# Performance work log

Hardware: AMD Instinct MI355X
Metric: run time of the kernel (lower is better)

Reference implementation:

```python
import math
import jax, jax.numpy as jnp
import numpy as np

LAMBDA_INIT = 0.8
GN_EPS = 1e-5

B, H, S, D = 2, 16, 2048, 128  # batch, heads, seq, head_dim


def setup_inputs() -> dict:
    key = jax.random.key(0)
    ks = jax.random.split(key, 8)
    return {
        "q": jax.random.normal(ks[0], (B, H, S, 2 * D), dtype=jnp.float32),
        "k": jax.random.normal(ks[1], (B, H, S, 2 * D), dtype=jnp.float32),
        "v": jax.random.normal(ks[2], (B, H, S, D), dtype=jnp.float32),
        "lam_q1": jax.random.normal(ks[3], (D,), dtype=jnp.float32),
        "lam_q2": jax.random.normal(ks[4], (D,), dtype=jnp.float32),
        "lam_k1": jax.random.normal(ks[5], (D,), dtype=jnp.float32),
        "lam_k2": jax.random.normal(ks[6], (D,), dtype=jnp.float32),
        "gn_weight": jnp.ones((H * D,), dtype=jnp.float32),
        "gn_bias": jnp.zeros((H * D,), dtype=jnp.float32),
    }


def reference(q, k, v, lam_q1, lam_q2, lam_k1, lam_k2, gn_weight, gn_bias):
    d = q.shape[-1] // 2
    scale = 1.0 / math.sqrt(d)
    Q1, Q2 = q[..., :d], q[..., d:]
    K1, K2 = k[..., :d], k[..., d:]
    # dual score matrices [B,H,S,S]
    w1 = jax.nn.softmax(jnp.einsum('bhsd,bhtd->bhst', Q1, K1) * scale, axis=-1)
    w2 = jax.nn.softmax(jnp.einsum('bhsd,bhtd->bhst', Q2, K2) * scale, axis=-1)
    lam = jnp.exp(jnp.dot(lam_q1, lam_k1)) - jnp.exp(jnp.dot(lam_q2, lam_k2)) + LAMBDA_INIT
    weights = w1 - lam * w2
    out = jnp.einsum('bhst,bhtd->bhsd', weights, v)  # [B,H,S,D]
    # GroupNorm(num_groups=H, num_channels=H*D) applied on [B, H*D, S]:
    # channel c = h*D + dd, normalization per (batch, head) over (D, S).
    mean = out.mean(axis=(2, 3), keepdims=True)
    var = out.var(axis=(2, 3), keepdims=True)
    normed = (out - mean) * jax.lax.rsqrt(var + GN_EPS)
    gamma = gn_weight.reshape(1, out.shape[1], 1, d)
    beta = gn_bias.reshape(1, out.shape[1], 1, d)
    return (normed * gamma + beta) * (1.0 - LAMBDA_INIT)
```

## Files before the change

kernel.cpp:

```cpp
#include <hip/hip_runtime.h>
#include <cstddef>

constexpr int B = 2, H = 16, S = 2048, D = 128;
constexpr int BH = B * H;
constexpr int TWOD = 2 * D;
constexpr int QTILE = 128;
constexpr int BC = 32;
constexpr int NKT = S / BC;
constexpr float SC2 = 0.08838834764831845f * 1.4426950408889634f;
constexpr float LAM_INIT = 0.8f;
constexpr float GN_EPS = 1e-5f;

typedef __attribute__((ext_vector_type(8))) short short8;
typedef __attribute__((ext_vector_type(4))) float f32x4;

__device__ __forceinline__ unsigned short f2b(float f) {
  unsigned int u = __float_as_uint(f);
  u += 0x7fffu + ((u >> 16) & 1u);
  return (unsigned short)(u >> 16);
}

__device__ __forceinline__ void async_copy16(const void* g, void* l) {
  typedef __attribute__((address_space(1))) const void gvoid;
  typedef __attribute__((address_space(3))) void lvoid;
  __builtin_amdgcn_global_load_lds((gvoid*)g, (lvoid*)l, 16, 0, 0);
}

__global__ void lam_kernel(const float* __restrict__ lq1, const float* __restrict__ lq2,
                           const float* __restrict__ lk1, const float* __restrict__ lk2,
                           float* __restrict__ wsf) {
  __shared__ float r1[128], r2[128];
  int t = threadIdx.x;
  r1[t] = lq1[t] * lk1[t];
  r2[t] = lq2[t] * lk2[t];
  __syncthreads();
  if (t == 0) {
    float s1 = 0.f, s2 = 0.f;
    for (int i = 0; i < 128; ++i) { s1 += r1[i]; s2 += r2[i]; }
    wsf[0] = expf(s1) - expf(s2) + LAM_INIT;
  }
}

__global__ void convk_kernel(const float* __restrict__ src, unsigned short* __restrict__ dst) {
  size_t i = ((size_t)blockIdx.x * 256 + threadIdx.x) * 8;
  float4 a = *(const float4*)(src + i);
  float4 b = *(const float4*)(src + i + 4);
  unsigned short u[8];
  u[0] = f2b(a.x); u[1] = f2b(a.y); u[2] = f2b(a.z); u[3] = f2b(a.w);
  u[4] = f2b(b.x); u[5] = f2b(b.y); u[6] = f2b(b.z); u[7] = f2b(b.w);
  *(uint4*)(dst + i) = *(uint4*)u;
}

__global__ void vt_kernel(const float* __restrict__ v, unsigned short* __restrict__ vtg) {
  __shared__ float tile[64][129];
  const int bh = blockIdx.y, s0 = blockIdx.x * 64, t = threadIdx.x;
#pragma unroll
  for (int i = 0; i < 8; ++i) {
    int idx = t + i * 256;
    int row = idx >> 5, c4 = idx & 31;
    float4 f = *(const float4*)(v + ((size_t)bh * S + s0 + row) * D + c4 * 4);
    tile[row][c4 * 4 + 0] = f.x; tile[row][c4 * 4 + 1] = f.y;
    tile[row][c4 * 4 + 2] = f.z; tile[row][c4 * 4 + 3] = f.w;
  }
  __syncthreads();
#pragma unroll
  for (int i = 0; i < 4; ++i) {
    int c = t + i * 256;
    int d = c >> 3, k8 = c & 7;
    unsigned short u[8];
#pragma unroll
    for (int j = 0; j < 8; ++j) u[j] = f2b(tile[k8 * 8 + j][d]);
    *(uint4*)(vtg + ((size_t)bh * D + d) * S + s0 + k8 * 8) = *(uint4*)u;
  }
}

__global__ __launch_bounds__(256, 2)
void attn_kernel(const float* __restrict__ q, const unsigned short* __restrict__ kbf,
                 const unsigned short* __restrict__ vtg,
                 float* __restrict__ wsf, float* __restrict__ out) {
  __shared__ __attribute__((aligned(16))) unsigned short Ks[2][32][256];
  __shared__ __attribute__((aligned(16))) unsigned short Vt[2][128][40];
  __shared__ __attribute__((aligned(16))) unsigned short Pa[4][2][32][40];
  __shared__ float sred[4][2];

  const int bh = blockIdx.x, qb = blockIdx.y;
  const int q0 = qb * QTILE;
  const int tid = threadIdx.x;
  const int wave = tid >> 6, lane = tid & 63;
  const int quad = lane >> 4, l16 = lane & 15;
  const float lam = wsf[0];

  short8 qf[2][2][4];
#pragma unroll
  for (int mt = 0; mt < 2; ++mt) {
    int qrow = q0 + wave * 32 + mt * 16 + l16;
    const float* qr = q + ((size_t)bh * S + qrow) * TWOD;
#pragma unroll
    for (int st = 0; st < 2; ++st)
#pragma unroll
      for (int ks = 0; ks < 4; ++ks) {
        const float* p = qr + st * D + ks * 32 + quad * 8;
        float4 f0 = *(const float4*)p;
        float4 f1 = *(const float4*)(p + 4);
        short8 v8;
        v8[0] = (short)f2b(f0.x); v8[1] = (short)f2b(f0.y);
        v8[2] = (short)f2b(f0.z); v8[3] = (short)f2b(f0.w);
        v8[4] = (short)f2b(f1.x); v8[5] = (short)f2b(f1.y);
        v8[6] = (short)f2b(f1.z); v8[7] = (short)f2b(f1.w);
        qf[mt][st][ks] = v8;
      }
  }

  const unsigned short* kbase = kbf + (size_t)bh * S * (size_t)TWOD;
  int goff[4];
#pragma unroll
  for (int i = 0; i < 4; ++i) {
    int L = i * 256 + tid;
    int row = L >> 5, cp = L & 31;
    int g = cp ^ (row & 7);
    goff[i] = row * 256 + g * 8;
  }
  const unsigned short* vbase = vtg + (size_t)bh * D * (size_t)S;
  const int vd0 = tid >> 2, vcp = tid & 3;

  f32x4 acc[2][2][8];
#pragma unroll
  for (int mt = 0; mt < 2; ++mt)
#pragma unroll
    for (int st = 0; st < 2; ++st)
#pragma unroll
      for (int n = 0; n < 8; ++n) acc[mt][st][n] = (f32x4){0.f, 0.f, 0.f, 0.f};
  float lacc[2][2][4];
#pragma unroll
  for (int mt = 0; mt < 2; ++mt)
#pragma unroll
    for (int st = 0; st < 2; ++st)
#pragma unroll
      for (int r = 0; r < 4; ++r) lacc[mt][st][r] = 0.f;

  const int pa_rd_off = (quad ^ ((l16 >> 2) & 3)) * 8;

  auto qk = [&](int st, int kb, f32x4 (&sa)[2][2]) {
#pragma unroll
    for (int nt = 0; nt < 2; ++nt) {
      const int row = nt * 16 + l16;
      const int rx = row & 7;
#pragma unroll
      for (int ks = 0; ks < 4; ++ks) {
        const int pos = (st * 16 + ks * 4 + quad) ^ rx;
        const short8 kf = *(const short8*)&Ks[kb][row][pos * 8];
        sa[0][nt] = __builtin_amdgcn_mfma_f32_16x16x32_bf16(qf[0][st][ks], kf, sa[0][nt], 0, 0, 0);
        sa[1][nt] = __builtin_amdgcn_mfma_f32_16x16x32_bf16(qf[1][st][ks], kf, sa[1][nt], 0, 0, 0);
      }
    }
  };
  auto pexp = [&](int st, f32x4 (&sa)[2][2]) {
#pragma unroll
    for (int mt = 0; mt < 2; ++mt)
#pragma unroll
      for (int nt = 0; nt < 2; ++nt)
#pragma unroll
        for (int r = 0; r < 4; ++r) {
          float p = __builtin_amdgcn_exp2f(sa[mt][nt][r] * SC2);
          lacc[mt][st][r] += p;
          int colp = (((nt * 2) + (l16 >> 3)) ^ quad) * 8 + (l16 & 7);
          Pa[wave][st][mt * 16 + quad * 4 + r][colp] = f2b(p);
        }
  };
  auto pv = [&](int st, const short8 (&paf)[2], const short8 (&vf)[8]) {
#pragma unroll
    for (int nt8 = 0; nt8 < 8; ++nt8)
#pragma unroll
      for (int mt = 0; mt < 2; ++mt)
        acc[mt][st][nt8] = __builtin_amdgcn_mfma_f32_16x16x32_bf16(paf[mt], vf[nt8], acc[mt][st][nt8], 0, 0, 0);
  };

  {
    const uint4 z = {0u, 0u, 0u, 0u};
    unsigned short* pz = &Pa[0][0][0][0];
    for (int i = tid; i < 1280; i += 256) *(uint4*)(pz + i * 8) = z;
    unsigned short* vz = &Vt[1][0][0];
    for (int i = tid; i < 640; i += 256) *(uint4*)(vz + i * 8) = z;
#pragma unroll
    for (int i = 0; i < 4; ++i)
      async_copy16(kbase + goff[i], &Ks[0][0][0] + (i * 256 + tid) * 8);
    uint4 v0 = *(const uint4*)(vbase + (size_t)vd0 * S + vcp * 8);
    uint4 v1 = *(const uint4*)(vbase + (size_t)(vd0 + 64) * S + vcp * 8);
    *(uint4*)&Vt[0][vd0][vcp * 8] = v0;
    *(uint4*)&Vt[0][vd0 + 64][vcp * 8] = v1;
  }
  __syncthreads();

  for (int t = 0; t < NKT; ++t) {
    const int kbuf = t & 1;
    const int pvbuf = kbuf ^ 1;

    short8 paf[2][2], vf[8];
#pragma unroll
    for (int st = 0; st < 2; ++st)
#pragma unroll
      for (int mt = 0; mt < 2; ++mt)
        paf[st][mt] = *(const short8*)&Pa[wave][st][mt * 16 + l16][pa_rd_off];
#pragma unroll
    for (int nt8 = 0; nt8 < 8; ++nt8)
      vf[nt8] = *(const short8*)&Vt[pvbuf][nt8 * 16 + l16][quad * 8];

    const bool pre = (t + 1 < NKT);
    uint4 vr0, vr1;
    if (pre) {
      const unsigned short* vp = vbase + (t + 1) * BC + vcp * 8;
      vr0 = *(const uint4*)(vp + (size_t)vd0 * S);
      vr1 = *(const uint4*)(vp + (size_t)(vd0 + 64) * S);
      const unsigned short* kp = kbase + (size_t)(t + 1) * BC * TWOD;
      unsigned short* ldsb = &Ks[pvbuf][0][0];
#pragma unroll
      for (int i = 0; i < 4; ++i)
        async_copy16(kp + goff[i], ldsb + (i * 256 + tid) * 8);
    }

    f32x4 sa0[2][2], sa1[2][2];
#pragma unroll
    for (int mt = 0; mt < 2; ++mt)
#pragma unroll
      for (int nt = 0; nt < 2; ++nt) {
        sa0[mt][nt] = (f32x4){0.f, 0.f, 0.f, 0.f};
        sa1[mt][nt] = (f32x4){0.f, 0.f, 0.f, 0.f};
      }
    qk(0, kbuf, sa0);
    pv(0, paf[0], vf);
    pexp(0, sa0);
    qk(1, kbuf, sa1);
    pv(1, paf[1], vf);
    pexp(1, sa1);

    __syncthreads();
    if (pre) {
      *(uint4*)&Vt[pvbuf][vd0][vcp * 8] = vr0;
      *(uint4*)&Vt[pvbuf][vd0 + 64][vcp * 8] = vr1;
    }
  }

  {
    short8 paf[2][2], vf[8];
#pragma unroll
    for (int st = 0; st < 2; ++st)
#pragma unroll
      for (int mt = 0; mt < 2; ++mt)
        paf[st][mt] = *(const short8*)&Pa[wave][st][mt * 16 + l16][pa_rd_off];
#pragma unroll
    for (int nt8 = 0; nt8 < 8; ++nt8)
      vf[nt8] = *(const short8*)&Vt[1][nt8 * 16 + l16][quad * 8];
    pv(0, paf[0], vf);
    pv(1, paf[1], vf);
  }

#pragma unroll
  for (int mt = 0; mt < 2; ++mt)
#pragma unroll
    for (int st = 0; st < 2; ++st)
#pragma unroll
      for (int r = 0; r < 4; ++r) {
        float v = lacc[mt][st][r];
        v += __shfl_xor(v, 1, 16);
        v += __shfl_xor(v, 2, 16);
        v += __shfl_xor(v, 4, 16);
        v += __shfl_xor(v, 8, 16);
        lacc[mt][st][r] = v;
      }

  float sum = 0.f, ssq = 0.f;
#pragma unroll
  for (int mt = 0; mt < 2; ++mt) {
    float i1[4], i2[4];
#pragma unroll
    for (int r = 0; r < 4; ++r) {
      i1[r] = 1.f / lacc[mt][0][r];
      i2[r] = lam / lacc[mt][1][r];
    }
#pragma unroll
    for (int nt8 = 0; nt8 < 8; ++nt8)
#pragma unroll
      for (int r = 0; r < 4; ++r) {
        float o = acc[mt][0][nt8][r] * i1[r] - acc[mt][1][nt8][r] * i2[r];
        int row = q0 + wave * 32 + mt * 16 + quad * 4 + r;
        out[((size_t)bh * S + row) * D + nt8 * 16 + l16] = o;
        sum += o; ssq += o * o;
      }
  }
#pragma unroll
  for (int off = 32; off >= 1; off >>= 1) {
    sum += __shfl_xor(sum, off, 64);
    ssq += __shfl_xor(ssq, off, 64);
  }
  if (lane == 0) { sred[wave][0] = sum; sred[wave][1] = ssq; }
  __syncthreads();
  if (tid == 0) {
    float s0 = sred[0][0] + sred[1][0] + sred[2][0] + sred[3][0];
    float s1 = sred[0][1] + sred[1][1] + sred[2][1] + sred[3][1];
    int idx = bh * 16 + qb;
    wsf[64 + idx * 2] = s0;
    wsf[64 + idx * 2 + 1] = s1;
  }
}

__global__ void gn_kernel(float* __restrict__ out, const float* __restrict__ gw,
                          const float* __restrict__ gb, const float* __restrict__ wsf) {
  const int bh = blockIdx.x, part = blockIdx.y;
  const int h = bh & (H - 1);
  float sum = 0.f, ssq = 0.f;
  for (int j = 0; j < 16; ++j) {
    sum += wsf[64 + (bh * 16 + j) * 2];
    ssq += wsf[64 + (bh * 16 + j) * 2 + 1];
  }
  const float invn = 1.f / (float)(S * D);
  const float mean = sum * invn;
  const float var = ssq * invn - mean * mean;
  const float rstd = rsqrtf(var + GN_EPS);
  const float outscale = 1.f - LAM_INIT;
  const float4* g4 = (const float4*)(gw + h * D);
  const float4* b4 = (const float4*)(gb + h * D);
  float4* o4 = (float4*)(out + (size_t)bh * S * D);
  const int chunks_per = (S * D / 4) / 8;
  const int c0 = part * chunks_per;
  for (int c = c0 + threadIdx.x; c < c0 + chunks_per; c += 256) {
    float4 vv = o4[c];
    int d4 = c & 31;
    float4 g = g4[d4], bb = b4[d4];
    vv.x = ((vv.x - mean) * rstd * g.x + bb.x) * outscale;
    vv.y = ((vv.y - mean) * rstd * g.y + bb.y) * outscale;
    vv.z = ((vv.z - mean) * rstd * g.z + bb.z) * outscale;
    vv.w = ((vv.w - mean) * rstd * g.w + bb.w) * outscale;
    o4[c] = vv;
  }
}

extern "C" void kernel_launch(void* const* d_in, const int* in_sizes, int n_in,
                              void* d_out, int out_size, void* d_ws, size_t ws_size,
                              hipStream_t stream) {
  (void)in_sizes; (void)n_in; (void)out_size; (void)ws_size;
  const float* q   = (const float*)d_in[0];
  const float* k   = (const float*)d_in[1];
  const float* v   = (const float*)d_in[2];
  const float* lq1 = (const float*)d_in[3];
  const float* lq2 = (const float*)d_in[4];
  const float* lk1 = (const float*)d_in[5];
  const float* lk2 = (const float*)d_in[6];
  const float* gw  = (const float*)d_in[7];
  const float* gb  = (const float*)d_in[8];
  float* out = (float*)d_out;
  float* wsf = (float*)d_ws;
  unsigned short* vtg = (unsigned short*)((char*)d_ws + 8192);
  unsigned short* kbf = (unsigned short*)((char*)d_ws + 8192 + (size_t)BH * D * S * 2);

  lam_kernel<<<dim3(1), dim3(128), 0, stream>>>(lq1, lq2, lk1, lk2, wsf);
  convk_kernel<<<dim3(BH * S * TWOD / 2048), dim3(256), 0, stream>>>(k, kbf);
  vt_kernel<<<dim3(S / 64, BH), dim3(256), 0, stream>>>(v, vtg);
  attn_kernel<<<dim3(BH, S / QTILE), dim3(256), 0, stream>>>(q, kbf, vtg, wsf, out);
  gn_kernel<<<dim3(BH, 8), dim3(256), 0, stream>>>(out, gw, gb, wsf);
}
```

Baseline: 401.2 us.

## Fuse prep kernels, load V fragments directly from global, widen GroupNorm grid

Merges the lambda, K-conversion and V-transpose kernels into one prep kernel, which cuts two launches. The attention kernel no longer stages transposed V through a double-buffered LDS tile. Each lane now reads its bf16 V fragments straight from global (L2) memory every iteration, which frees LDS and drops the V store/sync work but exposes global load latency inside the loop. The GroupNorm kernel grid goes from 8 to 32 parts per head for more parallelism.

```diff
diff --git a/kernel.cpp b/kernel.cpp
--- a/kernel.cpp
+++ b/kernel.cpp
@@ -26,34 +26,43 @@
   __builtin_amdgcn_global_load_lds((gvoid*)g, (lvoid*)l, 16, 0, 0);
 }
 
-__global__ void lam_kernel(const float* __restrict__ lq1, const float* __restrict__ lq2,
-                           const float* __restrict__ lk1, const float* __restrict__ lk2,
-                           float* __restrict__ wsf) {
-  __shared__ float r1[128], r2[128];
-  int t = threadIdx.x;
-  r1[t] = lq1[t] * lk1[t];
-  r2[t] = lq2[t] * lk2[t];
-  __syncthreads();
-  if (t == 0) {
-    float s1 = 0.f, s2 = 0.f;
-    for (int i = 0; i < 128; ++i) { s1 += r1[i]; s2 += r2[i]; }
-    wsf[0] = expf(s1) - expf(s2) + LAM_INIT;
-  }
-}
-
-__global__ void convk_kernel(const float* __restrict__ src, unsigned short* __restrict__ dst) {
-  size_t i = ((size_t)blockIdx.x * 256 + threadIdx.x) * 8;
-  float4 a = *(const float4*)(src + i);
-  float4 b = *(const float4*)(src + i + 4);
-  unsigned short u[8];
-  u[0] = f2b(a.x); u[1] = f2b(a.y); u[2] = f2b(a.z); u[3] = f2b(a.w);
-  u[4] = f2b(b.x); u[5] = f2b(b.y); u[6] = f2b(b.z); u[7] = f2b(b.w);
-  *(uint4*)(dst + i) = *(uint4*)u;
-}
-
-__global__ void vt_kernel(const float* __restrict__ v, unsigned short* __restrict__ vtg) {
+__global__ void prep_kernel(const float* __restrict__ k, const float* __restrict__ v,
+                            const float* __restrict__ lq1, const float* __restrict__ lq2,
+                            const float* __restrict__ lk1, const float* __restrict__ lk2,
+                            unsigned short* __restrict__ kbf, unsigned short* __restrict__ vtg,
+                            float* __restrict__ wsf) {
   __shared__ float tile[64][129];
   const int bh = blockIdx.y, s0 = blockIdx.x * 64, t = threadIdx.x;
+
+  if (blockIdx.x == 0 && blockIdx.y == 0) {
+    if (t < 128) {
+      tile[0][t] = lq1[t] * lk1[t];
+      tile[1][t] = lq2[t] * lk2[t];
+    }
+    __syncthreads();
+    if (t == 0) {
+      float s1 = 0.f, s2 = 0.f;
+      for (int i = 0; i < 128; ++i) { s1 += tile[0][i]; s2 += tile[1][i]; }
+      wsf[0] = expf(s1) - expf(s2) + LAM_INIT;
+    }
+    __syncthreads();
+  }
+
+  {
+    const float* ks = k + ((size_t)bh * S + s0) * TWOD;
+    unsigned short* kd = kbf + ((size_t)bh * S + s0) * TWOD;
+#pragma unroll
+    for (int i = 0; i < 8; ++i) {
+      size_t off = (size_t)(i * 256 + t) * 8;
+      float4 a = *(const float4*)(ks + off);
+      float4 b2 = *(const float4*)(ks + off + 4);
+      unsigned short u[8];
+      u[0] = f2b(a.x); u[1] = f2b(a.y); u[2] = f2b(a.z); u[3] = f2b(a.w);
+      u[4] = f2b(b2.x); u[5] = f2b(b2.y); u[6] = f2b(b2.z); u[7] = f2b(b2.w);
+      *(uint4*)(kd + off) = *(uint4*)u;
+    }
+  }
+
 #pragma unroll
   for (int i = 0; i < 8; ++i) {
     int idx = t + i * 256;
@@ -79,7 +88,6 @@
                  const unsigned short* __restrict__ vtg,
                  float* __restrict__ wsf, float* __restrict__ out) {
   __shared__ __attribute__((aligned(16))) unsigned short Ks[2][32][256];
-  __shared__ __attribute__((aligned(16))) unsigned short Vt[2][128][40];
   __shared__ __attribute__((aligned(16))) unsigned short Pa[4][2][32][40];
   __shared__ float sred[4][2];
 
@@ -120,8 +128,7 @@
     int g = cp ^ (row & 7);
     goff[i] = row * 256 + g * 8;
   }
-  const unsigned short* vbase = vtg + (size_t)bh * D * (size_t)S;
-  const int vd0 = tid >> 2, vcp = tid & 3;
+  const unsigned short* vlane = vtg + ((size_t)bh * D + l16) * S + quad * 8;
 
   f32x4 acc[2][2][8];
 #pragma unroll
@@ -179,40 +186,32 @@
     const uint4 z = {0u, 0u, 0u, 0u};
     unsigned short* pz = &Pa[0][0][0][0];
     for (int i = tid; i < 1280; i += 256) *(uint4*)(pz + i * 8) = z;
-    unsigned short* vz = &Vt[1][0][0];
-    for (int i = tid; i < 640; i += 256) *(uint4*)(vz + i * 8) = z;
 #pragma unroll
     for (int i = 0; i < 4; ++i)
       async_copy16(kbase + goff[i], &Ks[0][0][0] + (i * 256 + tid) * 8);
-    uint4 v0 = *(const uint4*)(vbase + (size_t)vd0 * S + vcp * 8);
-    uint4 v1 = *(const uint4*)(vbase + (size_t)(vd0 + 64) * S + vcp * 8);
-    *(uint4*)&Vt[0][vd0][vcp * 8] = v0;
-    *(uint4*)&Vt[0][vd0 + 64][vcp * 8] = v1;
   }
   __syncthreads();
 
   for (int t = 0; t < NKT; ++t) {
     const int kbuf = t & 1;
-    const int pvbuf = kbuf ^ 1;
-
-    short8 paf[2][2], vf[8];
+    const int nbuf = kbuf ^ 1;
+
+    const int tv = (t == 0) ? 0 : (t - 1);
+    short8 vf[8];
+#pragma unroll
+    for (int nt8 = 0; nt8 < 8; ++nt8)
+      vf[nt8] = *(const short8*)(vlane + (size_t)(nt8 * 16) * S + tv * BC);
+
+    short8 paf[2][2];
 #pragma unroll
     for (int st = 0; st < 2; ++st)
 #pragma unroll
       for (int mt = 0; mt < 2; ++mt)
         paf[st][mt] = *(const short8*)&Pa[wave][st][mt * 16 + l16][pa_rd_off];
-#pragma unroll
-    for (int nt8 = 0; nt8 < 8; ++nt8)
-      vf[nt8] = *(const short8*)&Vt[pvbuf][nt8 * 16 + l16][quad * 8];
-
-    const bool pre = (t + 1 < NKT);
-    uint4 vr0, vr1;
-    if (pre) {
-      const unsigned short* vp = vbase + (t + 1) * BC + vcp * 8;
-      vr0 = *(const uint4*)(vp + (size_t)vd0 * S);
-      vr1 = *(const uint4*)(vp + (size_t)(vd0 + 64) * S);
+
+    if (t + 1 < NKT) {
       const unsigned short* kp = kbase + (size_t)(t + 1) * BC * TWOD;
-      unsigned short* ldsb = &Ks[pvbuf][0][0];
+      unsigned short* ldsb = &Ks[nbuf][0][0];
 #pragma unroll
       for (int i = 0; i < 4; ++i)
         async_copy16(kp + goff[i], ldsb + (i * 256 + tid) * 8);
@@ -234,22 +233,18 @@
     pexp(1, sa1);
 
     __syncthreads();
-    if (pre) {
-      *(uint4*)&Vt[pvbuf][vd0][vcp * 8] = vr0;
-      *(uint4*)&Vt[pvbuf][vd0 + 64][vcp * 8] = vr1;
-    }
   }
 
   {
     short8 paf[2][2], vf[8];
 #pragma unroll
+    for (int nt8 = 0; nt8 < 8; ++nt8)
+      vf[nt8] = *(const short8*)(vlane + (size_t)(nt8 * 16) * S + (NKT - 1) * BC);
+#pragma unroll
     for (int st = 0; st < 2; ++st)
 #pragma unroll
       for (int mt = 0; mt < 2; ++mt)
         paf[st][mt] = *(const short8*)&Pa[wave][st][mt * 16 + l16][pa_rd_off];
-#pragma unroll
-    for (int nt8 = 0; nt8 < 8; ++nt8)
-      vf[nt8] = *(const short8*)&Vt[1][nt8 * 16 + l16][quad * 8];
     pv(0, paf[0], vf);
     pv(1, paf[1], vf);
   }
@@ -320,7 +315,7 @@
   const float4* g4 = (const float4*)(gw + h * D);
   const float4* b4 = (const float4*)(gb + h * D);
   float4* o4 = (float4*)(out + (size_t)bh * S * D);
-  const int chunks_per = (S * D / 4) / 8;
+  const int chunks_per = (S * D / 4) / 32;
   const int c0 = part * chunks_per;
   for (int c = c0 + threadIdx.x; c < c0 + chunks_per; c += 256) {
     float4 vv = o4[c];
@@ -352,9 +347,7 @@
   unsigned short* vtg = (unsigned short*)((char*)d_ws + 8192);
   unsigned short* kbf = (unsigned short*)((char*)d_ws + 8192 + (size_t)BH * D * S * 2);
 
-  lam_kernel<<<dim3(1), dim3(128), 0, stream>>>(lq1, lq2, lk1, lk2, wsf);
-  convk_kernel<<<dim3(BH * S * TWOD / 2048), dim3(256), 0, stream>>>(k, kbf);
-  vt_kernel<<<dim3(S / 64, BH), dim3(256), 0, stream>>>(v, vtg);
+  prep_kernel<<<dim3(S / 64, BH), dim3(256), 0, stream>>>(k, v, lq1, lq2, lk1, lk2, kbf, vtg, wsf);
   attn_kernel<<<dim3(BH, S / QTILE), dim3(256), 0, stream>>>(q, kbf, vtg, wsf, out);
-  gn_kernel<<<dim3(BH, 8), dim3(256), 0, stream>>>(out, gw, gb, wsf);
-}
+  gn_kernel<<<dim3(BH, 32), dim3(256), 0, stream>>>(out, gw, gb, wsf);
+}
```

Measured after the change: 617.7 us. 1.54x slower.
